# Kernel optimization log

Measured on AMD Instinct MI355X. Metric: run time of the kernel, lower is better.

The kernel has to match this reference:

```python
import jax, jax.numpy as jnp
import numpy as np


def setup_inputs() -> dict:
    key = jax.random.key(0)
    k1, k2 = jax.random.split(key)
    inputs = jax.random.normal(k1, (4, 128, 64, 64), dtype=jnp.float32)
    # binary hole mask (1 = known background, 0 = hole), broadcast over channels
    mask = jnp.round(jax.random.uniform(k2, (4, 1, 64, 64), dtype=jnp.float32))
    return {"inputs": inputs, "mask": mask}


def reference(inputs, mask):
    # SFFA contextual attention with 1x1 dynamic kernels.
    # Note: in the original torch code the 1x1 conv with padding=1 produces
    # border scores that conv_transpose2d with padding=1 crops away exactly,
    # so the math reduces to per-pixel matmul + softmax + matmul.
    bz, nc, h, w = inputs.shape
    N = h * w
    background = inputs * mask                              # [b, c, h, w]
    # dynamic kernels: one nc-dim vector per background pixel (patch)
    K = background.reshape(bz, nc, N).transpose(0, 2, 1) + 1e-7   # [b, N, c]
    Kn = K / jnp.sqrt(jnp.sum(K * K, axis=2, keepdims=True))      # l2-normalized
    feat = inputs.reshape(bz, nc, N)                        # [b, c, N]
    scores = jnp.einsum('bpc,bcn->bpn', Kn, feat)           # [b, N(patch), N(pixel)]
    attn = jax.nn.softmax(scores, axis=1)                   # softmax over patches p
    agg = jnp.einsum('bpc,bpn->bcn', K, attn).reshape(bz, nc, h, w)
    return background + agg * (1.0 - mask)
```

## Files before the change

### kernel.cpp

```cpp
#include <hip/hip_runtime.h>
#include <hip/hip_bf16.h>

typedef __attribute__((ext_vector_type(8))) short bf16x8;
typedef __attribute__((ext_vector_type(4))) float f32x4;

#define NPIX 4096
#define NC   128
#define RS128 0.08838834764831845f

__global__ __launch_bounds__(1024) void sffa_scan_copy(
    const float* __restrict__ mask, const float4* __restrict__ x4,
    int* __restrict__ prefBH, int* __restrict__ cnts, float4* __restrict__ out4)
{
    __shared__ int wsum[16];
    const int tid = threadIdx.x;
    if (blockIdx.x >= 4) {
        const int i0 = ((int)blockIdx.x - 4) * 2048 + tid;
        out4[i0] = x4[i0];
        out4[i0 + 1024] = x4[i0 + 1024];
        return;
    }
    const int b = blockIdx.x;
    const int lane = tid & 63, w = tid >> 6;
    float4 mv = *(const float4*)(mask + (size_t)b * NPIX + tid * 4);
    int f0 = mv.x < 0.5f ? 0x10000 : 1;
    int f1 = mv.y < 0.5f ? 0x10000 : 1;
    int f2 = mv.z < 0.5f ? 0x10000 : 1;
    int f3 = mv.w < 0.5f ? 0x10000 : 1;
    int tot = f0 + f1 + f2 + f3;
    int sc = tot;
    #pragma unroll
    for (int d = 1; d < 64; d <<= 1) { int t = __shfl_up(sc, d); if (lane >= d) sc += t; }
    if (lane == 63) wsum[w] = sc;
    __syncthreads();
    if (w == 0) {
        int v = (lane < 16) ? wsum[lane] : 0;
        int s = v;
        #pragma unroll
        for (int d = 1; d < 16; d <<= 1) { int t = __shfl_up(s, d); if (lane >= d) s += t; }
        if (lane < 16) wsum[lane] = s - v;
    }
    __syncthreads();
    int base = wsum[w] + sc - tot;
    int e0 = base, e1 = e0 + f0, e2 = e1 + f1, e3 = e2 + f2;
    *(int4*)(prefBH + (size_t)b * NPIX + tid * 4) = make_int4(e0, e1, e2, e3);
    if (tid == 1023) {
        int total = e3 + f3;
        cnts[b * 2]     = total & 0xffff;
        cnts[b * 2 + 1] = total >> 16;
    }
}

__global__ __launch_bounds__(1024) void sffa_prep(
    const float* __restrict__ x, const float* __restrict__ mask,
    const int* __restrict__ prefBH,
    ushort* __restrict__ KnW, ushort* __restrict__ QW, ushort* __restrict__ VtW,
    float* __restrict__ s0c, int* __restrict__ pixQ)
{
    __shared__ float xs[128][69];
    __shared__ float ms[64];
    __shared__ float rinv[64];
    __shared__ float ssum[64];
    __shared__ float2 part[16][64];
    __shared__ int se[64];
    __shared__ int bgn[64];
    __shared__ int tinfo[2];
    const int tid = threadIdx.x;
    const int b = blockIdx.x >> 6, nblk = blockIdx.x & 63;
    const int n0 = nblk * 64;
    const float* xb = x + (size_t)b * NC * NPIX;

    #pragma unroll
    for (int it = 0; it < 2; ++it) {
        int e4 = it * 1024 + tid;
        int c = e4 >> 4, n4 = (e4 & 15) * 4;
        float4 v = *(const float4*)(xb + (size_t)c * NPIX + n0 + n4);
        xs[c][n4+0] = v.x; xs[c][n4+1] = v.y; xs[c][n4+2] = v.z; xs[c][n4+3] = v.w;
    }
    if (tid < 16) {
        float4 mv = *(const float4*)(mask + (size_t)b * NPIX + n0 + tid * 4);
        ms[tid*4+0] = mv.x; ms[tid*4+1] = mv.y; ms[tid*4+2] = mv.z; ms[tid*4+3] = mv.w;
    }
    if (tid >= 960) {
        int j = tid - 960;
        se[j] = prefBH[(size_t)b * NPIX + n0 + j];
    }
    __syncthreads();
    {
        int p = tid & 63, qd = tid >> 6;
        float m = ms[p];
        float s2 = 0.f, s1 = 0.f;
        #pragma unroll
        for (int i = 0; i < 8; ++i) {
            float xv = xs[qd*8 + i][p];
            float k = fmaf(xv, m, 1e-7f);
            s2 = fmaf(k, k, s2);
            s1 += xv;
        }
        part[qd][p] = make_float2(s2, s1);
    }
    __syncthreads();
    if (tid < 64) {
        float s2 = 0.f, s1 = 0.f;
        #pragma unroll
        for (int k = 0; k < 16; ++k) { float2 t = part[k][tid]; s2 += t.x; s1 += t.y; }
        rinv[tid] = rsqrtf(s2);
        ssum[tid] = s1 * RS128;
    }
    __syncthreads();
    #pragma unroll
    for (int it = 0; it < 4; ++it) {
        int e2 = it * 1024 + tid;
        int n = e2 >> 6, cp = (e2 & 63) * 2;
        int pe = se[n];
        float x0 = xs[cp][n], x1 = xs[cp+1][n];
        if (ms[n] > 0.5f) {
            int slot = pe & 0xffff;
            float k0 = x0 + 1e-7f, k1 = x1 + 1e-7f;
            float r = rinv[n];
            __hip_bfloat162 kn;
            kn.x = __float2bfloat16(k0 * r); kn.y = __float2bfloat16(k1 * r);
            *(__hip_bfloat162*)(KnW + ((size_t)b * NPIX + slot) * NC + cp) = kn;
        } else {
            int slot = pe >> 16;
            __hip_bfloat162 q;
            q.x = __float2bfloat16(x0); q.y = __float2bfloat16(x1);
            *(__hip_bfloat162*)(QW + ((size_t)b * NPIX + slot) * NC + cp) = q;
        }
    }
    if (tid < 64) {
        if (ms[tid] < 0.5f) {
            int slot = se[tid] >> 16;
            s0c [(size_t)b * NPIX + slot] = ssum[tid];
            pixQ[(size_t)b * NPIX + slot] = n0 + tid;
        } else {
            bgn[(se[tid] & 0xffff) - (se[0] & 0xffff)] = tid;
        }
    }
    if (tid == 0) {
        tinfo[0] = se[0] & 0xffff;
        tinfo[1] = (se[63] & 0xffff) + (ms[63] > 0.5f ? 1 : 0) - (se[0] & 0xffff);
    }
    __syncthreads();
    {
        const int s0b = tinfo[0], nbg = tinfo[1];
        const int j = tid & 63, cg = tid >> 6;
        if (j < nbg) {
            int n = bgn[j];
            ushort* vcol = VtW + (size_t)b * NC * NPIX + s0b + j;
            #pragma unroll
            for (int cc = 0; cc < 8; ++cc) {
                int c = cg * 8 + cc;
                __hip_bfloat16 h = __float2bfloat16(xs[c][n] + 1e-7f);
                vcol[(size_t)c * NPIX] = *(ushort*)&h;
            }
        }
    }
}

#define L_BUF 32768
#define L_P   65536
#define L_ML  75776
#define L_SZ  76800

__global__ __launch_bounds__(512, 4) void sffa_attn(
    const ushort* __restrict__ KnW, const ushort* __restrict__ QW,
    const ushort* __restrict__ VtW, const int* __restrict__ cnts,
    ushort* __restrict__ partW, float* __restrict__ mlW, int KS)
{
    __shared__ __align__(16) char smem[L_SZ];
    const int tid  = threadIdx.x;
    const int w = tid >> 6, lane = tid & 63;
    const int l15 = lane & 15, g = lane >> 4;
    const int bx = (int)blockIdx.x;
    const int per = 64 * KS;
    const int b = bx / per;
    const int rem = bx - b * per;
    const int qblk = rem / KS, ks = rem - (rem / KS) * KS;
    const int q0 = qblk * 64;
    const int cntK = cnts[b * 2], cntQ = cnts[b * 2 + 1];
    if (q0 >= cntQ) return;
    const int blk = (b * 64 + qblk) * KS + ks;

    const int nk64 = (cntK + 63) >> 6;
    const int tpk  = (nk64 + KS - 1) / KS;
    const int t0   = ks * tpk;
    const int t1   = min(t0 + tpk, nk64);
    const int NTK  = t1 - t0;

    if (NTK <= 0) {
        unsigned* pz = (unsigned*)(partW + (size_t)blk * 8192);
        #pragma unroll
        for (int i = 0; i < 8; ++i) pz[i * 512 + tid] = 0u;
        if (tid < 64)
            *(float2*)(mlW + ((size_t)blk * 64 + tid) * 2) = make_float2(-1e30f, 0.f);
        return;
    }

    const int half = w >> 2;
    const int wq   = w & 3;
    const int kbase = t0 * 64;

    const ushort* Knb = KnW + (size_t)b * NPIX * NC;
    const ushort* Qb  = QW  + (size_t)b * NPIX * NC + (size_t)q0 * NC;
    const ushort* Vtb = VtW + (size_t)b * NC * NPIX;

    #pragma unroll
    for (int it = 0; it < 2; ++it) {
        int L = (it * 512 + tid) * 16;
        int row = L >> 8, col = L & 255;
        int4 v = *(const int4*)((const char*)Qb + L);
        *(int4*)(smem + row * 256 + (col ^ ((row & 15) << 4))) = v;
    }
    __syncthreads();
    bf16x8 qf[4];
    {
        int qrow = wq * 16 + l15;
        #pragma unroll
        for (int kc = 0; kc < 4; ++kc)
            qf[kc] = *(const bf16x8*)(smem + qrow * 256 + ((64*kc + 16*g) ^ (l15 << 4)));
    }
    __syncthreads();

    const int kOff = (tid >> 4) * 256 + (((tid & 15) * 16) ^ (((tid >> 4) & 15) << 4));
    const int cV = tid >> 3, sV = tid & 7;
    const int vOff = cV * 128 + ((sV * 16) ^ ((cV & 7) << 4));
    const int4* kgbase = (const int4*)(Knb + (size_t)kbase * NC);
    const ushort* vgbase = Vtb + (size_t)cV * NPIX + kbase + sV * 8;

    int4 pr0, pr1, pr2, pr3;
    pr0 = kgbase[tid]; pr1 = kgbase[512 + tid];
    pr2 = *(const int4*)(vgbase);
    pr3 = *(const int4*)(vgbase + (size_t)64 * NPIX);
    {
        char* base = smem;
        *(int4*)(base + kOff) = pr0;
        *(int4*)(base + kOff + 8192) = pr1;
        *(int4*)(base + 16384 + vOff) = pr2;
        *(int4*)(base + 16384 + vOff + 8192) = pr3;
    }
    if (NTK > 1) {
        pr0 = kgbase[1024 + tid]; pr1 = kgbase[1536 + tid];
        pr2 = *(const int4*)(vgbase + 64);
        pr3 = *(const int4*)(vgbase + (size_t)64 * NPIX + 64);
    }
    __syncthreads();

    f32x4 acc[8];
    const f32x4 fzero = {0.f, 0.f, 0.f, 0.f};
    #pragma unroll
    for (int i = 0; i < 8; ++i) acc[i] = fzero;
    float mrun = -1e30f, lrun = 0.f;
    char* Pw = smem + L_P + w * 1280;

    for (int kt = 0; kt < NTK; ++kt) {
        if (kt + 1 < NTK) {
            char* base = smem + ((kt + 1) & 1) * L_BUF;
            *(int4*)(base + kOff) = pr0;
            *(int4*)(base + kOff + 8192) = pr1;
            *(int4*)(base + 16384 + vOff) = pr2;
            *(int4*)(base + 16384 + vOff + 8192) = pr3;
        }
        if (kt + 2 < NTK) {
            pr0 = kgbase[(kt + 2) * 1024 + tid];
            pr1 = kgbase[(kt + 2) * 1024 + 512 + tid];
            pr2 = *(const int4*)(vgbase + (kt + 2) * 64);
            pr3 = *(const int4*)(vgbase + (size_t)64 * NPIX + (kt + 2) * 64);
        }
        char* bb = smem + (kt & 1) * L_BUF;
        f32x4 sa0 = fzero, sa1 = fzero;
        {
            const char* rb0 = bb + (half * 32 + l15) * 256;
            const char* rb1 = rb0 + 4096;
            const int sw = l15 << 4;
            __builtin_amdgcn_s_setprio(1);
            #pragma unroll
            for (int kc = 0; kc < 4; ++kc) {
                int off = (64 * kc + 16 * g) ^ sw;
                bf16x8 a0 = *(const bf16x8*)(rb0 + off);
                bf16x8 a1 = *(const bf16x8*)(rb1 + off);
                sa0 = __builtin_amdgcn_mfma_f32_16x16x32_bf16(a0, qf[kc], sa0, 0, 0, 0);
                sa1 = __builtin_amdgcn_mfma_f32_16x16x32_bf16(a1, qf[kc], sa1, 0, 0, 0);
            }
            __builtin_amdgcn_s_setprio(0);
        }
        {
            int kg0 = (t0 + kt) * 64;
            if (kg0 + 64 > cntK) {
                int kb = cntK - kg0;
                int kr = half * 32 + 4 * g;
                #pragma unroll
                for (int r = 0; r < 4; ++r) {
                    if (kr + r >= kb)      sa0[r] = -3e38f;
                    if (kr + 16 + r >= kb) sa1[r] = -3e38f;
                }
            }
        }
        float tmax = fmaxf(fmaxf(fmaxf(sa0[0], sa0[1]), fmaxf(sa0[2], sa0[3])),
                           fmaxf(fmaxf(sa1[0], sa1[1]), fmaxf(sa1[2], sa1[3])));
        tmax = fmaxf(tmax, __shfl_xor(tmax, 16));
        tmax = fmaxf(tmax, __shfl_xor(tmax, 32));
        bool grow = !__all(tmax <= mrun + 8.f);
        float mnew = grow ? fmaxf(mrun, tmax) : mrun;
        float p0[4], p1[4];
        float ts = 0.f;
        #pragma unroll
        for (int r = 0; r < 4; ++r) { p0[r] = __expf(sa0[r] - mnew); ts += p0[r]; }
        #pragma unroll
        for (int r = 0; r < 4; ++r) { p1[r] = __expf(sa1[r] - mnew); ts += p1[r]; }
        ts += __shfl_xor(ts, 16);
        ts += __shfl_xor(ts, 32);
        if (grow) {
            float sc = __expf(mrun - mnew);
            lrun = lrun * sc + ts;
            float scr[4];
            #pragma unroll
            for (int r = 0; r < 4; ++r) scr[r] = __shfl(sc, 4 * g + r);
            #pragma unroll
            for (int ct = 0; ct < 8; ++ct) {
                acc[ct][0] *= scr[0]; acc[ct][1] *= scr[1];
                acc[ct][2] *= scr[2]; acc[ct][3] *= scr[3];
            }
            mrun = mnew;
        } else {
            lrun += ts;
        }
        union { __hip_bfloat162 h; unsigned u; } ua0, ua1, ub0, ub1;
        ua0.h.x = __float2bfloat16(p0[0]); ua0.h.y = __float2bfloat16(p0[1]);
        ua1.h.x = __float2bfloat16(p0[2]); ua1.h.y = __float2bfloat16(p0[3]);
        ub0.h.x = __float2bfloat16(p1[0]); ub0.h.y = __float2bfloat16(p1[1]);
        ub1.h.x = __float2bfloat16(p1[2]); ub1.h.y = __float2bfloat16(p1[3]);
        *(int2*)(Pw + l15 * 80 +      8 * g) = make_int2((int)ua0.u, (int)ua1.u);
        *(int2*)(Pw + l15 * 80 + 32 + 8 * g) = make_int2((int)ub0.u, (int)ub1.u);
        bf16x8 pf = *(const bf16x8*)(Pw + l15 * 80 + 16 * g);
        {
            const char* vb = bb + 16384;
            __builtin_amdgcn_s_setprio(1);
            #pragma unroll
            for (int ct = 0; ct < 8; ++ct) {
                int c = 16 * ct + l15;
                bf16x8 vf = *(const bf16x8*)(vb + c * 128 +
                                             ((64 * half + 16 * g) ^ ((c & 7) << 4)));
                acc[ct] = __builtin_amdgcn_mfma_f32_16x16x32_bf16(pf, vf, acc[ct], 0, 0, 0);
            }
            __builtin_amdgcn_s_setprio(0);
        }
        __syncthreads();
    }

    float* ma = (float*)(smem + L_ML);
    float* la = ma + 64; float* mb = la + 64; float* lb = mb + 64;
    const int q = wq * 16 + l15;
    if (g == 0) {
        if (half == 0) { ma[q] = mrun; la[q] = lrun; }
        else           { mb[q] = mrun; lb[q] = lrun; }
    }
    __syncthreads();
    float* agg = (float*)smem;
    {
        float mstar = fmaxf(ma[q], mb[q]);
        float f = __expf(mrun - mstar);
        float fr[4];
        #pragma unroll
        for (int r = 0; r < 4; ++r) fr[r] = __shfl(f, 4 * g + r);
        if (half == 1) {
            #pragma unroll
            for (int ct = 0; ct < 8; ++ct) {
                int c = 16 * ct + l15;
                #pragma unroll
                for (int r = 0; r < 4; ++r)
                    agg[c * 68 + wq * 16 + 4 * g + r] = acc[ct][r] * fr[r];
            }
        }
        __syncthreads();
        if (half == 0) {
            #pragma unroll
            for (int ct = 0; ct < 8; ++ct) {
                int c = 16 * ct + l15;
                #pragma unroll
                for (int r = 0; r < 4; ++r) {
                    int idx = c * 68 + wq * 16 + 4 * g + r;
                    agg[idx] = acc[ct][r] * fr[r] + agg[idx];
                }
            }
        }
    }
    __syncthreads();
    if (tid < 64) {
        float M = fmaxf(ma[tid], mb[tid]);
        float ls = la[tid] * __expf(ma[tid] - M) + lb[tid] * __expf(mb[tid] - M);
        *(float2*)(mlW + ((size_t)blk * 64 + tid) * 2) = make_float2(M, ls);
    }
    ushort* pdst = partW + (size_t)blk * 8192;
    #pragma unroll
    for (int it = 0; it < 8; ++it) {
        int idx = it * 512 + tid;
        int c = idx >> 5, n2 = (idx & 31) * 2;
        __hip_bfloat162 h;
        h.x = __float2bfloat16(agg[c * 68 + n2]);
        h.y = __float2bfloat16(agg[c * 68 + n2 + 1]);
        *(__hip_bfloat162*)(pdst + c * 64 + n2) = h;
    }
}

__global__ __launch_bounds__(256) void sffa_comb(
    const ushort* __restrict__ partW, const float* __restrict__ mlW,
    const float* __restrict__ s0c, const int* __restrict__ pixQ,
    const int* __restrict__ cnts, float* __restrict__ out, int KS)
{
    __shared__ float wgtL[4][64];
    __shared__ int pixnL[64];
    const int tid = threadIdx.x;
    const int bx = blockIdx.x;
    const int b = bx >> 8, qb = (bx >> 2) & 63, ch = bx & 3;
    const int cntK = cnts[b * 2], cntQ = cnts[b * 2 + 1];
    if (qb * 64 >= cntQ) return;
    const int blkbase = (b * 64 + qb) * KS;
    const float m0f = (float)(NPIX - cntK);

    if (tid < 64) {
        int slot = qb * 64 + tid;
        int pix = -1;
        if (slot < cntQ) {
            pix = pixQ[(size_t)b * NPIX + slot];
            float s0 = s0c[(size_t)b * NPIX + slot];
            float M = s0;
            float2 mls[4];
            #pragma unroll
            for (int k = 0; k < 4; ++k) {
                if (k < KS) {
                    mls[k] = *(const float2*)(mlW + ((size_t)(blkbase + k) * 64 + tid) * 2);
                    M = fmaxf(M, mls[k].x);
                }
            }
            float L = m0f * __expf(s0 - M);
            #pragma unroll
            for (int k = 0; k < 4; ++k)
                if (k < KS) L += mls[k].y * __expf(mls[k].x - M);
            float Li = 1.f / L;
            #pragma unroll
            for (int k = 0; k < 4; ++k)
                if (k < KS) wgtL[k][tid] = __expf(mls[k].x - M) * Li;
        }
        pixnL[tid] = pix;
    }
    __syncthreads();

    float* ob = out + (size_t)b * NC * NPIX;
    const ushort* pb = partW + (size_t)blkbase * 8192;
    {
        int cl = tid >> 3, grp = tid & 7;
        int c = ch * 32 + cl;
        float v[8] = {0.f,0.f,0.f,0.f,0.f,0.f,0.f,0.f};
        #pragma unroll
        for (int k = 0; k < 4; ++k) {
            if (k < KS) {
                ushort u[8];
                *(int4*)u = *(const int4*)(pb + (size_t)k * 8192 + c * 64 + grp * 8);
                #pragma unroll
                for (int j = 0; j < 8; ++j)
                    v[j] = fmaf(__uint_as_float((unsigned)u[j] << 16),
                                wgtL[k][grp * 8 + j], v[j]);
            }
        }
        #pragma unroll
        for (int j = 0; j < 8; ++j) {
            int pix = pixnL[grp * 8 + j];
            if (pix >= 0) ob[(size_t)c * NPIX + pix] = v[j];
        }
    }
}

extern "C" void kernel_launch(void* const* d_in, const int* in_sizes, int n_in,
                              void* d_out, int out_size, void* d_ws, size_t ws_size,
                              hipStream_t stream) {
    const float* x    = (const float*)d_in[0];
    const float* mask = (const float*)d_in[1];
    char* ws = (char*)d_ws;
    const size_t MBy = 1024 * 1024;
    const size_t KBy = 1024;

    ushort* KnW = (ushort*)(ws);
    ushort* QW  = (ushort*)(ws + 4 * MBy);
    ushort* VtW = (ushort*)(ws + 8 * MBy);

    size_t need4 = 12 * MBy + 4 * 4 * MBy + 1 * MBy;
    int KS = (ws_size >= need4) ? 4 : 2;
    ushort* partW = (ushort*)(ws + 12 * MBy);
    char* tail = ws + 12 * MBy + (size_t)KS * 4 * MBy;
    float* mlW    = (float*)(tail);
    int*   prefBH = (int*)(tail + 512 * KBy);
    float* s0c    = (float*)(tail + 576 * KBy);
    int*   pixQ   = (int*)(tail + 640 * KBy);
    int*   cnts   = (int*)(tail + 704 * KBy);

    sffa_scan_copy<<<260, 1024, 0, stream>>>(mask, (const float4*)x, prefBH, cnts,
                                             (float4*)d_out);
    sffa_prep <<<256, 1024, 0, stream>>>(x, mask, prefBH, KnW, QW, VtW, s0c, pixQ);
    sffa_attn <<<4 * 64 * KS, 512, 0, stream>>>(KnW, QW, VtW, cnts, partW, mlW, KS);
    sffa_comb <<<4 * 64 * 4, 256, 0, stream>>>(partW, mlW, s0c, pixQ, cnts,
                                               (float*)d_out, KS);
}
```

Measured before the change: 56.47 us.

## Fuse mask prefix scan and output copy into prep kernel

Removes the separate scan/copy kernel. Each prep block now recomputes the per-batch prefix count of background/hole pixels before its tile by reducing the full mask, and writes the input tile to the output while loading it. This saves one kernel launch and the extra read of x, at the cost of every block redundantly scanning a 4096-entry mask.

```diff
diff --git a/kernel.cpp b/kernel.cpp
--- a/kernel.cpp
+++ b/kernel.cpp
@@ -8,54 +8,11 @@
 #define NC   128
 #define RS128 0.08838834764831845f
 
-__global__ __launch_bounds__(1024) void sffa_scan_copy(
-    const float* __restrict__ mask, const float4* __restrict__ x4,
-    int* __restrict__ prefBH, int* __restrict__ cnts, float4* __restrict__ out4)
-{
-    __shared__ int wsum[16];
-    const int tid = threadIdx.x;
-    if (blockIdx.x >= 4) {
-        const int i0 = ((int)blockIdx.x - 4) * 2048 + tid;
-        out4[i0] = x4[i0];
-        out4[i0 + 1024] = x4[i0 + 1024];
-        return;
-    }
-    const int b = blockIdx.x;
-    const int lane = tid & 63, w = tid >> 6;
-    float4 mv = *(const float4*)(mask + (size_t)b * NPIX + tid * 4);
-    int f0 = mv.x < 0.5f ? 0x10000 : 1;
-    int f1 = mv.y < 0.5f ? 0x10000 : 1;
-    int f2 = mv.z < 0.5f ? 0x10000 : 1;
-    int f3 = mv.w < 0.5f ? 0x10000 : 1;
-    int tot = f0 + f1 + f2 + f3;
-    int sc = tot;
-    #pragma unroll
-    for (int d = 1; d < 64; d <<= 1) { int t = __shfl_up(sc, d); if (lane >= d) sc += t; }
-    if (lane == 63) wsum[w] = sc;
-    __syncthreads();
-    if (w == 0) {
-        int v = (lane < 16) ? wsum[lane] : 0;
-        int s = v;
-        #pragma unroll
-        for (int d = 1; d < 16; d <<= 1) { int t = __shfl_up(s, d); if (lane >= d) s += t; }
-        if (lane < 16) wsum[lane] = s - v;
-    }
-    __syncthreads();
-    int base = wsum[w] + sc - tot;
-    int e0 = base, e1 = e0 + f0, e2 = e1 + f1, e3 = e2 + f2;
-    *(int4*)(prefBH + (size_t)b * NPIX + tid * 4) = make_int4(e0, e1, e2, e3);
-    if (tid == 1023) {
-        int total = e3 + f3;
-        cnts[b * 2]     = total & 0xffff;
-        cnts[b * 2 + 1] = total >> 16;
-    }
-}
-
 __global__ __launch_bounds__(1024) void sffa_prep(
     const float* __restrict__ x, const float* __restrict__ mask,
-    const int* __restrict__ prefBH,
     ushort* __restrict__ KnW, ushort* __restrict__ QW, ushort* __restrict__ VtW,
-    float* __restrict__ s0c, int* __restrict__ pixQ)
+    float* __restrict__ s0c, int* __restrict__ pixQ, int* __restrict__ cnts,
+    float* __restrict__ out)
 {
     __shared__ float xs[128][69];
     __shared__ float ms[64];
@@ -65,10 +22,12 @@
     __shared__ int se[64];
     __shared__ int bgn[64];
     __shared__ int tinfo[2];
+    __shared__ int wredP[16], wredT[16];
     const int tid = threadIdx.x;
     const int b = blockIdx.x >> 6, nblk = blockIdx.x & 63;
     const int n0 = nblk * 64;
     const float* xb = x + (size_t)b * NC * NPIX;
+    float* ob = out + (size_t)b * NC * NPIX;
 
     #pragma unroll
     for (int it = 0; it < 2; ++it) {
@@ -76,14 +35,55 @@
         int c = e4 >> 4, n4 = (e4 & 15) * 4;
         float4 v = *(const float4*)(xb + (size_t)c * NPIX + n0 + n4);
         xs[c][n4+0] = v.x; xs[c][n4+1] = v.y; xs[c][n4+2] = v.z; xs[c][n4+3] = v.w;
+        *(float4*)(ob + (size_t)c * NPIX + n0 + n4) = v;
     }
     if (tid < 16) {
         float4 mv = *(const float4*)(mask + (size_t)b * NPIX + n0 + tid * 4);
         ms[tid*4+0] = mv.x; ms[tid*4+1] = mv.y; ms[tid*4+2] = mv.z; ms[tid*4+3] = mv.w;
     }
-    if (tid >= 960) {
-        int j = tid - 960;
-        se[j] = prefBH[(size_t)b * NPIX + n0 + j];
+    {
+        const int lane = tid & 63, w = tid >> 6;
+        float4 mv = *(const float4*)(mask + (size_t)b * NPIX + tid * 4);
+        int f0 = mv.x < 0.5f ? 0x10000 : 1;
+        int f1 = mv.y < 0.5f ? 0x10000 : 1;
+        int f2 = mv.z < 0.5f ? 0x10000 : 1;
+        int f3 = mv.w < 0.5f ? 0x10000 : 1;
+        int p0 = tid * 4;
+        int pre = 0, tot = f0 + f1 + f2 + f3;
+        if (p0 + 0 < n0) pre += f0;
+        if (p0 + 1 < n0) pre += f1;
+        if (p0 + 2 < n0) pre += f2;
+        if (p0 + 3 < n0) pre += f3;
+        #pragma unroll
+        for (int d = 1; d < 64; d <<= 1) {
+            pre += __shfl_xor(pre, d);
+            tot += __shfl_xor(tot, d);
+        }
+        if (lane == 0) { wredP[w] = pre; wredT[w] = tot; }
+    }
+    __syncthreads();
+    if (tid < 64) {
+        int vP = (tid < 16) ? wredP[tid] : 0;
+        int vT = (tid < 16) ? wredT[tid] : 0;
+        #pragma unroll
+        for (int d = 1; d < 16; d <<= 1) {
+            vP += __shfl_xor(vP, d);
+            vT += __shfl_xor(vT, d);
+        }
+        int base  = __shfl(vP, 0);
+        int total = __shfl(vT, 0);
+        if (tid == 0 && nblk == 0) {
+            cnts[b * 2]     = total & 0xffff;
+            cnts[b * 2 + 1] = total >> 16;
+        }
+        int f = ms[tid] > 0.5f ? 1 : 0x10000;
+        int s = f;
+        #pragma unroll
+        for (int d = 1; d < 64; d <<= 1) {
+            int t = __shfl_up(s, d);
+            if (tid >= d) s += t;
+        }
+        se[tid] = base + s - f;
     }
     __syncthreads();
     {
@@ -489,14 +489,12 @@
     ushort* partW = (ushort*)(ws + 12 * MBy);
     char* tail = ws + 12 * MBy + (size_t)KS * 4 * MBy;
     float* mlW    = (float*)(tail);
-    int*   prefBH = (int*)(tail + 512 * KBy);
     float* s0c    = (float*)(tail + 576 * KBy);
     int*   pixQ   = (int*)(tail + 640 * KBy);
     int*   cnts   = (int*)(tail + 704 * KBy);
 
-    sffa_scan_copy<<<260, 1024, 0, stream>>>(mask, (const float4*)x, prefBH, cnts,
-                                             (float4*)d_out);
-    sffa_prep <<<256, 1024, 0, stream>>>(x, mask, prefBH, KnW, QW, VtW, s0c, pixQ);
+    sffa_prep <<<256, 1024, 0, stream>>>(x, mask, KnW, QW, VtW, s0c, pixQ, cnts,
+                                         (float*)d_out);
     sffa_attn <<<4 * 64 * KS, 512, 0, stream>>>(KnW, QW, VtW, cnts, partW, mlW, KS);
     sffa_comb <<<4 * 64 * 4, 256, 0, stream>>>(partW, mlW, s0c, pixQ, cnts,
                                                (float*)d_out, KS);
```

New measurement: 53.38 us. 1.06x faster.
